# Kernel tuning notes

Measured on AMD Instinct MI355X. Metric: run time of the kernel, lower is better.

## Reference

```python
import jax, jax.numpy as jnp
import numpy as np

DIM = 1024; H = 16; DH = 64; L = 32; W = 8; E = 4  # ext_len = window_size//2
SEQ = 4096; B = 4
LN_EPS = 1e-5


def _ln(x, g, b):
    m = x.mean(-1, keepdims=True)
    v = ((x - m) ** 2).mean(-1, keepdims=True)
    return (x - m) / jnp.sqrt(v + LN_EPS) * g + b


def _split(x):  # (b,s,H*dh) -> (b,H,s,dh)
    b, s, _ = x.shape
    return x.reshape(b, s, H, DH).transpose(0, 2, 1, 3)


def _forward(query, Wq, bq, Wk, bk, Wv, bv, Wo, bo, g_l, b_l, g_s, b_s, Wd, bd):
    X = query.transpose(1, 0, 2)  # (b,s,d); s already multiple of W so no pad
    b, s, _ = X.shape
    Q = _split(X @ Wq + bq) * (1.0 / np.sqrt(DH))           # (b,H,s,dh)
    K = _split(_ln(X @ Wk + bk, g_l, b_l))
    V = _split(_ln(X @ Wv + bv, g_l, b_l))

    # landmark compression: softmax over sequence dim (no padding -> no mask)
    head_scores = jax.nn.softmax(X @ Wd + bd, axis=1)       # (b,s,H*L)
    hs = head_scores.reshape(b, s, H, L).transpose(0, 2, 3, 1)  # (b,H,L,s)
    Kc = jnp.einsum('bhls,bhsd->bhld', hs, K)
    Vc = jnp.einsum('bhls,bhsd->bhld', hs, V)
    # dual_ln_s applied over the flattened head dim, per landmark
    Kc = _split(_ln(Kc.transpose(0, 2, 1, 3).reshape(b, L, DIM), g_s, b_s))
    Vc = _split(_ln(Vc.transpose(0, 2, 1, 3).reshape(b, L, DIM), g_s, b_s))

    attn_compress = jnp.einsum('bhsd,bhld->bhsl', Q, Kc)    # (b,H,s,L)

    # sliding window band (v2): pad E on each side, tile into groups of W
    g = s // W
    band = W + 2 * E  # 16
    idx = jnp.arange(g)[:, None] * W + jnp.arange(band)[None, :]  # (g,band)
    K_pad = jnp.pad(K, ((0, 0), (0, 0), (E, E), (0, 0)))
    K_tiles = K_pad[:, :, idx, :]                           # (b,H,g,band,dh)
    Q_tiles = Q.reshape(b, H, g, W, DH)
    win = jnp.einsum('bhgwd,bhgkd->bhgwk', Q_tiles, K_tiles)
    valid = jnp.pad(jnp.ones((s,), bool), (E, E))[idx]      # (g,band) halo=False
    win = jnp.where(valid[None, None, :, None, :], win, -jnp.inf)
    win_flat = win.reshape(b, H, s, band)

    all_attn = jax.nn.softmax(jnp.concatenate([attn_compress, win_flat], -1), axis=-1)
    C = jnp.einsum('bhsl,bhld->bhsd', all_attn[..., :L], Vc)
    win_probs = all_attn[..., L:].reshape(b, H, g, W, band)
    V_pad = jnp.pad(V, ((0, 0), (0, 0), (E, E), (0, 0)))
    V_tiles = V_pad[:, :, idx, :]
    C = C + jnp.einsum('bhgwk,bhgkd->bhgwd', win_probs, V_tiles).reshape(b, H, s, DH)

    out = C.transpose(0, 2, 1, 3).reshape(b, s, DIM) @ Wo + bo
    return out.transpose(1, 0, 2)  # (s,b,d)


def setup_inputs() -> dict:
    key = jax.random.key(0)
    ks = jax.random.split(key, 7)
    sc = 0.02
    return {
        'query': jax.random.normal(ks[0], (SEQ, B, DIM), jnp.float32),
        'Wq': jax.random.normal(ks[1], (DIM, DIM), jnp.float32) * sc,
        'bq': jnp.zeros((DIM,), jnp.float32),
        'Wk': jax.random.normal(ks[2], (DIM, DIM), jnp.float32) * sc,
        'bk': jnp.zeros((DIM,), jnp.float32),
        'Wv': jax.random.normal(ks[3], (DIM, DIM), jnp.float32) * sc,
        'bv': jnp.zeros((DIM,), jnp.float32),
        'Wo': jax.random.normal(ks[4], (DIM, DIM), jnp.float32) * sc,
        'bo': jnp.zeros((DIM,), jnp.float32),
        'g_l': jnp.ones((DIM,), jnp.float32),
        'b_l': jnp.zeros((DIM,), jnp.float32),
        'g_s': jnp.ones((DIM,), jnp.float32),
        'b_s': jnp.zeros((DIM,), jnp.float32),
        'Wd': jax.random.normal(ks[5], (DIM, H * L), jnp.float32) * sc,
        'bd': jnp.zeros((H * L,), jnp.float32),
    }


def reference(query, Wq, bq, Wk, bk, Wv, bv, Wo, bo, g_l, b_l, g_s, b_s, Wd, bd):
    return _forward(query, Wq, bq, Wk, bk, Wv, bv, Wo, bo, g_l, b_l, g_s, b_s, Wd, bd)
```

## Files before the change

kernel.cpp:

```cpp
#include <hip/hip_runtime.h>
#include <cstddef>
#include <cstdint>

#define DIMC 1024
#define HC   16
#define DHC  64
#define LC   32
#define WC   8
#define EC   4
#define SEQC 4096
#define BC   4
#define MTOT 16384

typedef __attribute__((ext_vector_type(8))) __bf16 bf16x8;
typedef __attribute__((ext_vector_type(4))) float f32x4;

__device__ inline unsigned short f2b(float f) {
  unsigned int u = __float_as_uint(f);
  u += 0x7fff + ((u >> 16) & 1);
  return (unsigned short)(u >> 16);
}
__device__ inline float b2f(unsigned short u) {
  return __uint_as_float(((unsigned int)u) << 16);
}

__device__ inline void gll16(const void* g, void* l) {
  __builtin_amdgcn_global_load_lds(
      (__attribute__((address_space(1))) void*)g,
      (__attribute__((address_space(3))) void*)l, 16, 0, 0);
}

__global__ __launch_bounds__(256) void conv_rows(const float* __restrict__ src,
    unsigned short* __restrict__ dst) {
  int r = blockIdx.x;
  int sr = ((r & 4095) << 2) | (r >> 12);
  const float4* s = (const float4*)(src + (size_t)sr * 1024);
  ushort4* d = (ushort4*)(dst + (size_t)r * 1024);
  int t = threadIdx.x;
  float4 v = s[t];
  d[t] = make_ushort4(f2b(v.x), f2b(v.y), f2b(v.z), f2b(v.w));
}

__global__ __launch_bounds__(256) void conv_wT_all(
    const float* __restrict__ Wq, const float* __restrict__ Wk,
    const float* __restrict__ Wv, const float* __restrict__ Wd,
    const float* __restrict__ Wo, unsigned short* __restrict__ wAll,
    unsigned short* __restrict__ woT) {
  __shared__ float tile[32][33];
  int z = blockIdx.z;
  const float* W = (z == 0) ? Wq : (z == 1) ? Wk : (z == 2) ? Wv
                   : (z == 3) ? Wd : Wo;
  unsigned short* WT = (z == 4) ? woT : (wAll + (size_t)z * 1048576);
  int N = (z == 3) ? 512 : 1024;
  int n0 = blockIdx.x * 32, k0 = blockIdx.y * 32;
  if (n0 >= N) return;
  int t = threadIdx.x;
  int tr = t >> 5, tc = t & 31;
#pragma unroll
  for (int i = 0; i < 4; ++i)
    tile[tr + i * 8][tc] = W[(size_t)(k0 + tr + i * 8) * N + n0 + tc];
  __syncthreads();
#pragma unroll
  for (int i = 0; i < 4; ++i)
    WT[(size_t)(n0 + tr + i * 8) * 1024 + k0 + tc] = f2b(tile[tc][tr + i * 8]);
}

__global__ __launch_bounds__(512, 2) void gemm256(
    const unsigned short* __restrict__ A, const unsigned short* __restrict__ BT,
    const float* __restrict__ b0, const float* __restrict__ b1,
    const float* __restrict__ b2, const float* __restrict__ b3,
    unsigned short* __restrict__ o0, unsigned short* __restrict__ o1,
    unsigned short* __restrict__ o2, float* __restrict__ oy,
    float* __restrict__ outf, int mode) {
  extern __shared__ char smb[];
  unsigned short* smu = (unsigned short*)smb;
  int t = threadIdx.x;
  int w = t >> 6, lane = t & 63;
  int m = lane & 15, q4 = lane >> 4;
  int wr = (w >> 2) * 128, wc = (w & 3) * 64;
  int id = blockIdx.x;
  int xcd = id & 7, jj0 = id >> 3;
  int rowT = xcd * 8 + (jj0 & 7), colT = jj0 >> 3;
  int rowBase = rowT * 256, nBase = colT * 256;

  int srow = t >> 2;
  int gsw = ((t & 3) ^ ((t >> 3) & 3)) * 8;
  const unsigned short* gA0 = A + (size_t)(rowBase + srow) * 1024 + gsw;
  const unsigned short* gA1 = A + (size_t)(rowBase + 128 + srow) * 1024 + gsw;
  const unsigned short* gB0 = BT + (size_t)(nBase + srow) * 1024 + gsw;
  const unsigned short* gB1 = BT + (size_t)(nBase + 128 + srow) * 1024 + gsw;
  int ldsP0 = w * 1024;
  int ldsP1 = 8192 + w * 1024;
  int sx = (q4 ^ ((m >> 1) & 3)) * 8;
  f32x4 acc[8][4] = {};

#define STAGE5(kt_, c_)                                              \
  {                                                                  \
    int kc_ = (kt_) * 32;                                            \
    gll16(gA0 + kc_, smb + (c_)*16384 + ldsP0);                      \
    gll16(gA1 + kc_, smb + (c_)*16384 + ldsP1);                      \
    gll16(gB0 + kc_, smb + 32768 + (c_)*16384 + ldsP0);              \
    gll16(gB1 + kc_, smb + 32768 + (c_)*16384 + ldsP1);              \
  }

  STAGE5(0, 0);
  STAGE5(1, 1);
  asm volatile("s_waitcnt vmcnt(4)" ::: "memory");
  __builtin_amdgcn_s_barrier();
  __builtin_amdgcn_sched_barrier(0);

  for (int kt = 0; kt < 32; ++kt) {
    int c = kt & 1;
    const unsigned short* Au = smu + c * 8192;
    const unsigned short* Bu = smu + 16384 + c * 8192;
    bf16x8 bf[4];
#pragma unroll
    for (int jj = 0; jj < 4; ++jj)
      bf[jj] = *(const bf16x8*)(Bu + (wc + jj * 16 + m) * 32 + sx);
#pragma unroll
    for (int ip = 0; ip < 4; ++ip) {
      bf16x8 af0 = *(const bf16x8*)(Au + (wr + (ip * 2) * 16 + m) * 32 + sx);
      bf16x8 af1 =
          *(const bf16x8*)(Au + (wr + (ip * 2 + 1) * 16 + m) * 32 + sx);
      __builtin_amdgcn_s_setprio(1);
#pragma unroll
      for (int jj = 0; jj < 4; ++jj)
        acc[ip * 2][jj] = __builtin_amdgcn_mfma_f32_16x16x32_bf16(
            af0, bf[jj], acc[ip * 2][jj], 0, 0, 0);
#pragma unroll
      for (int jj = 0; jj < 4; ++jj)
        acc[ip * 2 + 1][jj] = __builtin_amdgcn_mfma_f32_16x16x32_bf16(
            af1, bf[jj], acc[ip * 2 + 1][jj], 0, 0, 0);
      __builtin_amdgcn_s_setprio(0);
    }
    if (kt == 31) break;
    __builtin_amdgcn_s_barrier();
    if (kt < 30) {
      STAGE5(kt + 2, c);
      asm volatile("s_waitcnt vmcnt(4)" ::: "memory");
    } else {
      asm volatile("s_waitcnt vmcnt(0)" ::: "memory");
    }
    __builtin_amdgcn_s_barrier();
    __builtin_amdgcn_sched_barrier(0);
  }
  __syncthreads();

  int segBase = nBase + wc;
  if (mode == 1) {
#pragma unroll
    for (int jj = 0; jj < 4; ++jj) {
      float bvv = b0[segBase + jj * 16 + m];
#pragma unroll
      for (int i = 0; i < 8; ++i)
#pragma unroll
        for (int r = 0; r < 4; ++r) {
          int rr = rowBase + wr + i * 16 + q4 * 4 + r;
          int orow = ((rr & 4095) << 2) | (rr >> 12);
          outf[(size_t)orow * 1024 + segBase + jj * 16 + m] =
              acc[i][jj][r] + bvv;
        }
    }
    return;
  }
  int seg = segBase >> 10;
  if (seg == 3) {
    int lc = segBase - 3072;
#pragma unroll
    for (int jj = 0; jj < 4; ++jj) {
      float bvv = b3[lc + jj * 16 + m];
#pragma unroll
      for (int i = 0; i < 8; ++i)
#pragma unroll
        for (int r = 0; r < 4; ++r)
          oy[(size_t)(rowBase + wr + i * 16 + q4 * 4 + r) * 512 + lc +
             jj * 16 + m] = acc[i][jj][r] + bvv;
    }
    return;
  }
  const float* bp = (seg == 0) ? b0 : (seg == 1) ? b1 : b2;
  unsigned short* ob = (seg == 0) ? o0 : (seg == 1) ? o1 : o2;
  float scl = (seg == 0) ? 0.125f : 1.0f;
  int lc0 = nBase & 1023;
#pragma unroll
  for (int h = 0; h < 2; ++h) {
    if ((w >> 2) == h) {
#pragma unroll
      for (int jj = 0; jj < 4; ++jj) {
        float bvv = bp[lc0 + wc + jj * 16 + m];
#pragma unroll
        for (int i = 0; i < 8; ++i)
#pragma unroll
          for (int r = 0; r < 4; ++r)
            smu[(i * 16 + q4 * 4 + r) * 264 + wc + jj * 16 + m] =
                f2b((acc[i][jj][r] + bvv) * scl);
      }
    }
    __syncthreads();
#pragma unroll
    for (int rd = 0; rd < 8; ++rd) {
      int idx = rd * 512 + t;
      int row = idx >> 5, cs = (idx & 31) * 8;
      uint4 v = *(const uint4*)(smu + row * 264 + cs);
      *(uint4*)(ob + (size_t)(rowBase + h * 128 + row) * 1024 + lc0 + cs) = v;
    }
    __syncthreads();
  }
}

__global__ __launch_bounds__(256) void ln_bf(unsigned short* __restrict__ buf,
    const float* __restrict__ g, const float* __restrict__ b) {
  int row = blockIdx.x;
  unsigned short* p = buf + (size_t)row * 1024;
  int tid = threadIdx.x;
  ushort4 u4 = ((const ushort4*)p)[tid];
  float x0 = b2f(u4.x), x1 = b2f(u4.y), x2 = b2f(u4.z), x3 = b2f(u4.w);
  float s = x0 + x1 + x2 + x3;
  float ss = x0 * x0 + x1 * x1 + x2 * x2 + x3 * x3;
#pragma unroll
  for (int off = 32; off > 0; off >>= 1) {
    s += __shfl_down(s, off);
    ss += __shfl_down(ss, off);
  }
  __shared__ float sred[8], ssred[8];
  int wave = tid >> 6, lane = tid & 63;
  if (lane == 0) { sred[wave] = s; ssred[wave] = ss; }
  __syncthreads();
  if (tid == 0) {
    float S = 0, SS = 0;
    for (int w = 0; w < 4; ++w) { S += sred[w]; SS += ssred[w]; }
    float m = S * (1.0f / 1024.0f);
    float v = SS * (1.0f / 1024.0f) - m * m;
    sred[0] = m;
    ssred[0] = rsqrtf(v + 1e-5f);
  }
  __syncthreads();
  float m = sred[0], rinv = ssred[0];
  float4 gg = ((const float4*)g)[tid];
  float4 bb = ((const float4*)b)[tid];
  ushort4 y;
  y.x = f2b((x0 - m) * rinv * gg.x + bb.x);
  y.y = f2b((x1 - m) * rinv * gg.y + bb.y);
  y.z = f2b((x2 - m) * rinv * gg.z + bb.z);
  y.w = f2b((x3 - m) * rinv * gg.w + bb.w);
  ((ushort4*)p)[tid] = y;
}

__global__ __launch_bounds__(256) void col_part(const float* __restrict__ yd,
    float* __restrict__ pm, float* __restrict__ ps) {
  int cg = blockIdx.x, b = blockIdx.y, sc = blockIdx.z;
  int t = threadIdx.x;
  int lane = t & 63, grp = t >> 6;
  const float* base = yd + (size_t)b * 4096 * 512 + (size_t)(sc * 256) * 512 +
                      cg * 64 + lane;
  float m = -1e30f, s = 0.f;
  for (int r = grp; r < 256; r += 4) {
    float x = base[(size_t)r * 512];
    float mn = fmaxf(m, x);
    s = s * expf(m - mn) + expf(x - mn);
    m = mn;
  }
  __shared__ float mS[4][64], sS[4][64];
  mS[grp][lane] = m;
  sS[grp][lane] = s;
  __syncthreads();
  if (grp == 0) {
    float M = mS[0][lane], S = sS[0][lane];
#pragma unroll
    for (int k = 1; k < 4; ++k) {
      float m2 = mS[k][lane], s2 = sS[k][lane];
      float Mn = fmaxf(M, m2);
      S = S * expf(M - Mn) + s2 * expf(m2 - Mn);
      M = Mn;
    }
    int col = cg * 64 + lane;
    pm[((size_t)(b * 512 + col)) * 16 + sc] = M;
    ps[((size_t)(b * 512 + col)) * 16 + sc] = S;
  }
}

__global__ __launch_bounds__(256) void col_combine(const float* __restrict__ pm,
    const float* __restrict__ ps, float* __restrict__ stats) {
  int idx = blockIdx.x * 256 + threadIdx.x;
  float M = -1e30f, S = 0.f;
#pragma unroll
  for (int sc = 0; sc < 16; ++sc) {
    float m2 = pm[(size_t)idx * 16 + sc], s2 = ps[(size_t)idx * 16 + sc];
    float Mn = fmaxf(M, m2);
    S = S * expf(M - Mn) + s2 * expf(m2 - Mn);
    M = Mn;
  }
  stats[(size_t)idx * 2] = M;
  stats[(size_t)idx * 2 + 1] = 1.0f / S;
}

#define NCHUNK 32
#define SCH    128
__global__ __launch_bounds__(256) void compress(const float* __restrict__ yd,
    const float* __restrict__ stats, const unsigned short* __restrict__ kbuf,
    const unsigned short* __restrict__ vbuf, float* __restrict__ kcp,
    float* __restrict__ vcp) {
  int c = blockIdx.x, h = blockIdx.y, b = blockIdx.z;
  int tid = threadIdx.x;
  int dq = tid & 15;
  int lp = tid >> 4;
  __shared__ float mxS[32], isS[32];
  __shared__ float pS[16][32];
  __shared__ float KfS[16][64];
  __shared__ float VfS[16][64];
  if (tid < 32) {
    mxS[tid] = stats[(size_t)(b * 512 + h * 32 + tid) * 2];
    isS[tid] = stats[(size_t)(b * 512 + h * 32 + tid) * 2 + 1];
  }
  __syncthreads();
  f32x4 aK0 = {}, aK1 = {}, aV0 = {}, aV1 = {};
  int s0 = c * SCH;
  for (int sc = 0; sc < SCH; sc += 16) {
    int bs = b * 4096 + s0 + sc;
    {
      int sl = tid >> 4;
      int l2 = (tid & 15) * 2;
      const float2 yv =
          *(const float2*)(yd + ((size_t)(bs + sl)) * 512 + h * 32 + l2);
      pS[sl][l2] = expf(yv.x - mxS[l2]) * isS[l2];
      pS[sl][l2 + 1] = expf(yv.y - mxS[l2 + 1]) * isS[l2 + 1];
      size_t roff = ((size_t)(bs + sl)) * 1024 + h * 64 + (tid & 15) * 4;
      ushort4 ku = *(const ushort4*)(kbuf + roff);
      ushort4 vu = *(const ushort4*)(vbuf + roff);
      f32x4 kf, vf;
      kf[0] = b2f(ku.x); kf[1] = b2f(ku.y); kf[2] = b2f(ku.z); kf[3] = b2f(ku.w);
      vf[0] = b2f(vu.x); vf[1] = b2f(vu.y); vf[2] = b2f(vu.z); vf[3] = b2f(vu.w);
      *(f32x4*)&KfS[sl][(tid & 15) * 4] = kf;
      *(f32x4*)&VfS[sl][(tid & 15) * 4] = vf;
    }
    __syncthreads();
#pragma unroll
    for (int sl = 0; sl < 16; ++sl) {
      float p0 = pS[sl][lp * 2];
      float p1 = pS[sl][lp * 2 + 1];
      const f32x4 kk = *(const f32x4*)&KfS[sl][dq * 4];
      const f32x4 vv = *(const f32x4*)&VfS[sl][dq * 4];
#pragma unroll
      for (int q = 0; q < 4; ++q) {
        aK0[q] += p0 * kk[q];
        aK1[q] += p1 * kk[q];
        aV0[q] += p0 * vv[q];
        aV1[q] += p1 * vv[q];
      }
    }
    __syncthreads();
  }
  size_t o0 = ((((size_t)c * 4 + b) * 16 + h) * 32 + (lp * 2)) * 64 + dq * 4;
  *(f32x4*)&kcp[o0] = aK0;
  *(f32x4*)&kcp[o0 + 64] = aK1;
  *(f32x4*)&vcp[o0] = aV0;
  *(f32x4*)&vcp[o0 + 64] = aV1;
}

__global__ __launch_bounds__(256) void ln_compress(const float* __restrict__ kcp,
    const float* __restrict__ vcp, const float* __restrict__ g_s,
    const float* __restrict__ b_s, float* __restrict__ kc_ln,
    float* __restrict__ vc_ln) {
  int row = blockIdx.x;
  int b = row >> 5, l = row & 31;
  const float* part = blockIdx.y ? vcp : kcp;
  float* outp = blockIdx.y ? vc_ln : kc_ln;
  int tid = threadIdx.x;
  int h = tid >> 4, d4 = (tid & 15) * 4;
  size_t base = (((size_t)b * 16 + h) * 32 + l) * 64 + d4;
  f32x4 x = {};
#pragma unroll
  for (int cch = 0; cch < NCHUNK; ++cch) {
    const f32x4 v = *(const f32x4*)&part[base + (size_t)cch * 131072];
#pragma unroll
    for (int q = 0; q < 4; ++q) x[q] += v[q];
  }
  float lsum = x[0] + x[1] + x[2] + x[3];
  float lss = x[0] * x[0] + x[1] * x[1] + x[2] * x[2] + x[3] * x[3];
#pragma unroll
  for (int off = 32; off > 0; off >>= 1) {
    lsum += __shfl_down(lsum, off);
    lss += __shfl_down(lss, off);
  }
  __shared__ float red[8], red2[8];
  int wave = tid >> 6, lane = tid & 63;
  if (lane == 0) { red[wave] = lsum; red2[wave] = lss; }
  __syncthreads();
  if (tid == 0) {
    float S = 0, SS = 0;
    for (int w = 0; w < 4; ++w) { S += red[w]; SS += red2[w]; }
    float m = S * (1.0f / 1024.0f);
    float v = SS * (1.0f / 1024.0f) - m * m;
    red[0] = m;
    red2[0] = rsqrtf(v + 1e-5f);
  }
  __syncthreads();
  float m = red[0], rinv = red2[0];
  int j = tid * 4;
  const float4 gg = *(const float4*)(g_s + j);
  const float4 bb = *(const float4*)(b_s + j);
  float4 yo;
  yo.x = (x[0] - m) * rinv * gg.x + bb.x;
  yo.y = (x[1] - m) * rinv * gg.y + bb.y;
  yo.z = (x[2] - m) * rinv * gg.z + bb.z;
  yo.w = (x[3] - m) * rinv * gg.w + bb.w;
  *(float4*)(outp + (size_t)row * 1024 + j) = yo;
}

__global__ __launch_bounds__(256) void attention(unsigned short* __restrict__ qc,
    const unsigned short* __restrict__ kbuf,
    const unsigned short* __restrict__ vbuf,
    const float* __restrict__ kc_ln, const float* __restrict__ vc_ln) {
  int qt = blockIdx.x, h = blockIdx.y, b = blockIdx.z;
  int t = threadIdx.x;
  int l = t & 63, w = t >> 6;
  int lr16 = l & 15, q4 = l >> 4;
  int s0 = qt * 64, hoff = h * 64;

  __shared__ unsigned short regionA[12672];
  __shared__ unsigned short Vt[64 * 128];
  unsigned short* Qs = regionA;
  unsigned short* Ks = regionA + 64 * 72;
  unsigned short* Ps = regionA;
  unsigned short* Cs = regionA + 64 * 128;

#pragma unroll
  for (int it = 0; it < 2; ++it) {
    int sid = it * 256 + t;
    int row = sid >> 3, seg = sid & 7;
    uint4 v = *(const uint4*)(qc + ((size_t)(b * 4096 + s0 + row)) * 1024 +
                              hoff + seg * 8);
    *(uint4*)(Qs + row * 72 + seg * 8) = v;
  }
#pragma unroll
  for (int it = 0; it < 2; ++it) {
    int sid = it * 256 + t;
    int row = sid >> 4, s4 = sid & 15;
    float4 v = *(const float4*)(kc_ln + ((size_t)(b * 32 + row)) * 1024 +
                                hoff + s4 * 4);
    ushort4 u = make_ushort4(f2b(v.x), f2b(v.y), f2b(v.z), f2b(v.w));
    *(ushort4*)(Ks + row * 72 + s4 * 4) = u;
  }
#pragma unroll
  for (int it = 0; it < 3; ++it) {
    int sid = it * 256 + t;
    if (sid < 576) {
      int r = sid >> 3, seg = sid & 7;
      int pos = s0 - 4 + r;
      uint4 v = {0, 0, 0, 0};
      if (pos >= 0 && pos < 4096)
        v = *(const uint4*)(kbuf + ((size_t)(b * 4096 + pos)) * 1024 + hoff +
                            seg * 8);
      *(uint4*)(Ks + (32 + r) * 72 + seg * 8) = v;
    }
  }
#pragma unroll
  for (int it = 0; it < 8; ++it) {
    int d = t & 63;
    int k0 = (t >> 6) * 4 + it * 16;
    unsigned short vv[4];
#pragma unroll
    for (int i = 0; i < 4; ++i) {
      int kk = k0 + i;
      unsigned short x = 0;
      if (kk < 32) {
        x = f2b(vc_ln[((size_t)(b * 32 + kk)) * 1024 + hoff + d]);
      } else if (kk < 104) {
        int pos = s0 - 4 + (kk - 32);
        if (pos >= 0 && pos < 4096)
          x = vbuf[((size_t)(b * 4096 + pos)) * 1024 + hoff + d];
      }
      vv[i] = x;
    }
    *(ushort4*)(Vt + d * 128 + (k0 ^ ((d & 31) << 2))) = *(ushort4*)vv;
  }
  __syncthreads();

  int mbase = w * 16;
  bf16x8 aq[2];
#pragma unroll
  for (int ks = 0; ks < 2; ++ks)
    aq[ks] = *(const bf16x8*)(Qs + (mbase + lr16) * 72 + ks * 32 + q4 * 8);
  f32x4 S[7];
#pragma unroll
  for (int nb = 0; nb < 7; ++nb) {
    f32x4 acc = {};
#pragma unroll
    for (int ks = 0; ks < 2; ++ks) {
      bf16x8 bk =
          *(const bf16x8*)(Ks + (nb * 16 + lr16) * 72 + ks * 32 + q4 * 8);
      acc = __builtin_amdgcn_mfma_f32_16x16x32_bf16(aq[ks], bk, acc, 0, 0, 0);
    }
    S[nb] = acc;
  }

  float ex[7][4];
#pragma unroll
  for (int r = 0; r < 4; ++r) {
    int qrow = mbase + q4 * 4 + r;
    int g8 = (qrow >> 3) * 8;
    float m = -1e30f;
#pragma unroll
    for (int nb = 0; nb < 7; ++nb) {
      int col = nb * 16 + lr16;
      float v = S[nb][r];
      if (col >= 32) {
        int rw = col - 32;
        int pos = s0 - 4 + rw;
        bool ok = (rw >= g8) && (rw < g8 + 16) && (pos >= 0) && (pos < 4096);
        if (!ok) v = -INFINITY;
      }
      ex[nb][r] = v;
      m = fmaxf(m, v);
    }
    m = fmaxf(m, __shfl_xor(m, 1));
    m = fmaxf(m, __shfl_xor(m, 2));
    m = fmaxf(m, __shfl_xor(m, 4));
    m = fmaxf(m, __shfl_xor(m, 8));
    float s = 0.f;
#pragma unroll
    for (int nb = 0; nb < 7; ++nb) {
      float e = expf(ex[nb][r] - m);
      ex[nb][r] = e;
      s += e;
    }
    s += __shfl_xor(s, 1);
    s += __shfl_xor(s, 2);
    s += __shfl_xor(s, 4);
    s += __shfl_xor(s, 8);
    float inv = 1.0f / s;
#pragma unroll
    for (int nb = 0; nb < 7; ++nb) ex[nb][r] *= inv;
  }
  __syncthreads();

  if (t < 128) {
    int q = t >> 1, blk = 14 + (t & 1);
    uint4 z = {0, 0, 0, 0};
    *(uint4*)(Ps + q * 128 + ((blk ^ (q & 7)) << 3)) = z;
  }
#pragma unroll
  for (int r = 0; r < 4; ++r) {
    int q = mbase + q4 * 4 + r;
#pragma unroll
    for (int nb = 0; nb < 7; ++nb) {
      int col = nb * 16 + lr16;
      int blk = col >> 3;
      Ps[q * 128 + ((blk ^ (q & 7)) << 3) + (col & 7)] = f2b(ex[nb][r]);
    }
  }
  __syncthreads();

  bf16x8 pa[4];
#pragma unroll
  for (int ks = 0; ks < 4; ++ks) {
    int q = mbase + lr16;
    int blk = ks * 4 + q4;
    pa[ks] = *(const bf16x8*)(Ps + q * 128 + ((blk ^ (q & 7)) << 3));
  }
#pragma unroll
  for (int nb = 0; nb < 4; ++nb) {
    f32x4 acc = {};
    int d = nb * 16 + lr16;
#pragma unroll
    for (int ks = 0; ks < 4; ++ks) {
      unsigned short vv[8];
#pragma unroll
      for (int jh = 0; jh < 2; ++jh) {
        int k4 = ks * 32 + q4 * 8 + jh * 4;
        *(ushort4*)(vv + jh * 4) =
            *(const ushort4*)(Vt + d * 128 + (k4 ^ ((d & 31) << 2)));
      }
      acc = __builtin_amdgcn_mfma_f32_16x16x32_bf16(pa[ks], *(const bf16x8*)vv,
                                                    acc, 0, 0, 0);
    }
#pragma unroll
    for (int r = 0; r < 4; ++r) {
      int row = mbase + q4 * 4 + r;
      Cs[row * 68 + d] = f2b(acc[r]);
    }
  }
  __syncthreads();

#pragma unroll
  for (int it = 0; it < 2; ++it) {
    int sid = it * 256 + t;
    int row = sid >> 3, seg = sid & 7;
    ushort4 a0 = *(const ushort4*)(Cs + row * 68 + seg * 8);
    ushort4 a1 = *(const ushort4*)(Cs + row * 68 + seg * 8 + 4);
    unsigned short u[8];
    *(ushort4*)u = a0;
    *(ushort4*)(u + 4) = a1;
    *(uint4*)(qc + ((size_t)(b * 4096 + s0 + row)) * 1024 + hoff + seg * 8) =
        *(uint4*)u;
  }
}

extern "C" void kernel_launch(void* const* d_in, const int* in_sizes, int n_in,
                              void* d_out, int out_size, void* d_ws,
                              size_t ws_size, hipStream_t stream) {
  const float* query = (const float*)d_in[0];
  const float* Wq = (const float*)d_in[1];
  const float* bq = (const float*)d_in[2];
  const float* Wk = (const float*)d_in[3];
  const float* bk = (const float*)d_in[4];
  const float* Wv = (const float*)d_in[5];
  const float* bv = (const float*)d_in[6];
  const float* Wo = (const float*)d_in[7];
  const float* bo = (const float*)d_in[8];
  const float* g_l = (const float*)d_in[9];
  const float* b_l = (const float*)d_in[10];
  const float* g_s = (const float*)d_in[11];
  const float* b_s = (const float*)d_in[12];
  const float* Wd = (const float*)d_in[13];
  const float* bd = (const float*)d_in[14];
  float* out = (float*)d_out;

  static bool attr_set = []() {
    hipFuncSetAttribute((const void*)gemm256,
                        hipFuncAttributeMaxDynamicSharedMemorySize, 135168);
    return true;
  }();
  (void)attr_set;

  unsigned short* qb = (unsigned short*)d_ws;
  unsigned short* kb = qb + 16777216;
  unsigned short* vb = kb + 16777216;
  unsigned short* xb = vb + 16777216;
  float* yd = (float*)(xb + 16777216);
  float* stats = yd + 8388608;
  float* col_pm = stats + 4096;
  float* col_ps = col_pm + 32768;
  float* kc_part = col_ps + 32768;
  float* vc_part = kc_part + 4194304;
  float* kc_ln = vc_part + 4194304;
  float* vc_ln = kc_ln + 131072;
  unsigned short* wAll = (unsigned short*)(vc_ln + 131072);
  unsigned short* woT = wAll + 3670016;

  dim3 blk(256);
  conv_rows<<<16384, blk, 0, stream>>>(query, xb);
  conv_wT_all<<<dim3(32, 32, 5), blk, 0, stream>>>(Wq, Wk, Wv, Wd, Wo,
                                                   wAll, woT);
  gemm256<<<896, dim3(512), 67584, stream>>>(xb, wAll, bq, bk, bv, bd,
                                             qb, kb, vb, yd, nullptr, 0);
  ln_bf<<<32768, blk, 0, stream>>>(kb, g_l, b_l);
  col_part<<<dim3(8, 4, 16), blk, 0, stream>>>(yd, col_pm, col_ps);
  col_combine<<<8, blk, 0, stream>>>(col_pm, col_ps, stats);
  compress<<<dim3(NCHUNK, 16, 4), blk, 0, stream>>>(yd, stats, kb, vb,
                                                    kc_part, vc_part);
  ln_compress<<<dim3(128, 2), blk, 0, stream>>>(kc_part, vc_part, g_s, b_s,
                                                kc_ln, vc_ln);
  attention<<<dim3(64, 16, 4), blk, 0, stream>>>(qb, kb, vb, kc_ln, vc_ln);
  gemm256<<<256, dim3(512), 67584, stream>>>(qb, woT, bo, nullptr, nullptr,
                                             nullptr, nullptr, nullptr,
                                             nullptr, nullptr, out, 1);
}
```

Measured before the change: 521.7 us.

## Shrink GEMM tile to 256x128 with triple-buffered LDS pipeline

Changes the bf16 MFMA GEMM from 256x256 tiles to 256x128 tiles, giving each wave a 64x64 sub-tile and doubling the grid size. It raises launch bounds to 4 blocks per CU and replaces double buffering with a three-stage LDS ring, issuing the next loads before compute and dropping one barrier per k-step. The aim is more occupancy and better latency hiding. In exchange, each block reuses less data, so total global traffic per FLOP goes up, and the epilogue now uses a single LDS pass.

```diff
diff --git a/kernel.cpp b/kernel.cpp
--- a/kernel.cpp
+++ b/kernel.cpp
@@ -65,7 +65,7 @@
     WT[(size_t)(n0 + tr + i * 8) * 1024 + k0 + tc] = f2b(tile[tc][tr + i * 8]);
 }
 
-__global__ __launch_bounds__(512, 2) void gemm256(
+__global__ __launch_bounds__(512, 4) void gemm128(
     const unsigned short* __restrict__ A, const unsigned short* __restrict__ BT,
     const float* __restrict__ b0, const float* __restrict__ b1,
     const float* __restrict__ b2, const float* __restrict__ b3,
@@ -77,67 +77,59 @@
   int t = threadIdx.x;
   int w = t >> 6, lane = t & 63;
   int m = lane & 15, q4 = lane >> 4;
-  int wr = (w >> 2) * 128, wc = (w & 3) * 64;
+  int wr = (w >> 1) * 64, wc = (w & 1) * 64;
   int id = blockIdx.x;
-  int xcd = id & 7, jj0 = id >> 3;
-  int rowT = xcd * 8 + (jj0 & 7), colT = jj0 >> 3;
-  int rowBase = rowT * 256, nBase = colT * 256;
+  int rowT = (id & 7) * 8 + ((id >> 3) & 7);
+  int colT = id >> 6;
+  int rowBase = rowT * 256, nBase = colT * 128;
 
   int srow = t >> 2;
   int gsw = ((t & 3) ^ ((t >> 3) & 3)) * 8;
   const unsigned short* gA0 = A + (size_t)(rowBase + srow) * 1024 + gsw;
   const unsigned short* gA1 = A + (size_t)(rowBase + 128 + srow) * 1024 + gsw;
   const unsigned short* gB0 = BT + (size_t)(nBase + srow) * 1024 + gsw;
-  const unsigned short* gB1 = BT + (size_t)(nBase + 128 + srow) * 1024 + gsw;
-  int ldsP0 = w * 1024;
-  int ldsP1 = 8192 + w * 1024;
+  int ldsW = w * 1024;
   int sx = (q4 ^ ((m >> 1) & 3)) * 8;
-  f32x4 acc[8][4] = {};
-
-#define STAGE5(kt_, c_)                                              \
-  {                                                                  \
-    int kc_ = (kt_) * 32;                                            \
-    gll16(gA0 + kc_, smb + (c_)*16384 + ldsP0);                      \
-    gll16(gA1 + kc_, smb + (c_)*16384 + ldsP1);                      \
-    gll16(gB0 + kc_, smb + 32768 + (c_)*16384 + ldsP0);              \
-    gll16(gB1 + kc_, smb + 32768 + (c_)*16384 + ldsP1);              \
-  }
-
-  STAGE5(0, 0);
-  STAGE5(1, 1);
-  asm volatile("s_waitcnt vmcnt(4)" ::: "memory");
+  f32x4 acc[4][4] = {};
+
+#define STAGE7(kt_, c_)                                          \
+  {                                                              \
+    int kc_ = (kt_) * 32;                                        \
+    gll16(gA0 + kc_, smb + (c_) * 24576 + ldsW);                 \
+    gll16(gA1 + kc_, smb + (c_) * 24576 + 8192 + ldsW);          \
+    gll16(gB0 + kc_, smb + (c_) * 24576 + 16384 + ldsW);         \
+  }
+
+  STAGE7(0, 0);
+  STAGE7(1, 1);
+  asm volatile("s_waitcnt vmcnt(3)" ::: "memory");
   __builtin_amdgcn_s_barrier();
   __builtin_amdgcn_sched_barrier(0);
 
   for (int kt = 0; kt < 32; ++kt) {
-    int c = kt & 1;
-    const unsigned short* Au = smu + c * 8192;
-    const unsigned short* Bu = smu + 16384 + c * 8192;
-    bf16x8 bf[4];
+    int c = kt % 3;
+    if (kt < 30) STAGE7(kt + 2, (kt + 2) % 3);
+    const unsigned short* Au = smu + c * 12288;
+    const unsigned short* Bu = smu + c * 12288 + 8192;
+    bf16x8 bfB[4];
 #pragma unroll
     for (int jj = 0; jj < 4; ++jj)
-      bf[jj] = *(const bf16x8*)(Bu + (wc + jj * 16 + m) * 32 + sx);
-#pragma unroll
-    for (int ip = 0; ip < 4; ++ip) {
-      bf16x8 af0 = *(const bf16x8*)(Au + (wr + (ip * 2) * 16 + m) * 32 + sx);
-      bf16x8 af1 =
-          *(const bf16x8*)(Au + (wr + (ip * 2 + 1) * 16 + m) * 32 + sx);
-      __builtin_amdgcn_s_setprio(1);
+      bfB[jj] = *(const bf16x8*)(Bu + (wc + jj * 16 + m) * 32 + sx);
+    bf16x8 afA[4];
+#pragma unroll
+    for (int mi = 0; mi < 4; ++mi)
+      afA[mi] = *(const bf16x8*)(Au + (wr + mi * 16 + m) * 32 + sx);
+    __builtin_amdgcn_s_setprio(1);
+#pragma unroll
+    for (int mi = 0; mi < 4; ++mi)
 #pragma unroll
       for (int jj = 0; jj < 4; ++jj)
-        acc[ip * 2][jj] = __builtin_amdgcn_mfma_f32_16x16x32_bf16(
-            af0, bf[jj], acc[ip * 2][jj], 0, 0, 0);
-#pragma unroll
-      for (int jj = 0; jj < 4; ++jj)
-        acc[ip * 2 + 1][jj] = __builtin_amdgcn_mfma_f32_16x16x32_bf16(
-            af1, bf[jj], acc[ip * 2 + 1][jj], 0, 0, 0);
-      __builtin_amdgcn_s_setprio(0);
-    }
+        acc[mi][jj] = __builtin_amdgcn_mfma_f32_16x16x32_bf16(
+            afA[mi], bfB[jj], acc[mi][jj], 0, 0, 0);
+    __builtin_amdgcn_s_setprio(0);
     if (kt == 31) break;
-    __builtin_amdgcn_s_barrier();
     if (kt < 30) {
-      STAGE5(kt + 2, c);
-      asm volatile("s_waitcnt vmcnt(4)" ::: "memory");
+      asm volatile("s_waitcnt vmcnt(3)" ::: "memory");
     } else {
       asm volatile("s_waitcnt vmcnt(0)" ::: "memory");
     }
@@ -146,35 +138,34 @@
   }
   __syncthreads();
 
-  int segBase = nBase + wc;
   if (mode == 1) {
 #pragma unroll
     for (int jj = 0; jj < 4; ++jj) {
-      float bvv = b0[segBase + jj * 16 + m];
-#pragma unroll
-      for (int i = 0; i < 8; ++i)
+      int col = nBase + wc + jj * 16 + m;
+      float bvv = b0[col];
+#pragma unroll
+      for (int mi = 0; mi < 4; ++mi)
 #pragma unroll
         for (int r = 0; r < 4; ++r) {
-          int rr = rowBase + wr + i * 16 + q4 * 4 + r;
+          int rr = rowBase + wr + mi * 16 + q4 * 4 + r;
           int orow = ((rr & 4095) << 2) | (rr >> 12);
-          outf[(size_t)orow * 1024 + segBase + jj * 16 + m] =
-              acc[i][jj][r] + bvv;
+          outf[(size_t)orow * 1024 + col] = acc[mi][jj][r] + bvv;
         }
     }
     return;
   }
-  int seg = segBase >> 10;
+  int seg = nBase >> 10;
   if (seg == 3) {
-    int lc = segBase - 3072;
+    int lc0 = nBase - 3072;
 #pragma unroll
     for (int jj = 0; jj < 4; ++jj) {
-      float bvv = b3[lc + jj * 16 + m];
-#pragma unroll
-      for (int i = 0; i < 8; ++i)
+      float bvv = b3[lc0 + wc + jj * 16 + m];
+#pragma unroll
+      for (int mi = 0; mi < 4; ++mi)
 #pragma unroll
         for (int r = 0; r < 4; ++r)
-          oy[(size_t)(rowBase + wr + i * 16 + q4 * 4 + r) * 512 + lc +
-             jj * 16 + m] = acc[i][jj][r] + bvv;
+          oy[(size_t)(rowBase + wr + mi * 16 + q4 * 4 + r) * 512 + lc0 + wc +
+             jj * 16 + m] = acc[mi][jj][r] + bvv;
     }
     return;
   }
@@ -183,28 +174,22 @@
   float scl = (seg == 0) ? 0.125f : 1.0f;
   int lc0 = nBase & 1023;
 #pragma unroll
-  for (int h = 0; h < 2; ++h) {
-    if ((w >> 2) == h) {
-#pragma unroll
-      for (int jj = 0; jj < 4; ++jj) {
-        float bvv = bp[lc0 + wc + jj * 16 + m];
-#pragma unroll
-        for (int i = 0; i < 8; ++i)
-#pragma unroll
-          for (int r = 0; r < 4; ++r)
-            smu[(i * 16 + q4 * 4 + r) * 264 + wc + jj * 16 + m] =
-                f2b((acc[i][jj][r] + bvv) * scl);
-      }
-    }
-    __syncthreads();
-#pragma unroll
-    for (int rd = 0; rd < 8; ++rd) {
-      int idx = rd * 512 + t;
-      int row = idx >> 5, cs = (idx & 31) * 8;
-      uint4 v = *(const uint4*)(smu + row * 264 + cs);
-      *(uint4*)(ob + (size_t)(rowBase + h * 128 + row) * 1024 + lc0 + cs) = v;
-    }
-    __syncthreads();
+  for (int jj = 0; jj < 4; ++jj) {
+    float bvv = bp[lc0 + wc + jj * 16 + m];
+#pragma unroll
+    for (int mi = 0; mi < 4; ++mi)
+#pragma unroll
+      for (int r = 0; r < 4; ++r)
+        smu[(wr + mi * 16 + q4 * 4 + r) * 136 + wc + jj * 16 + m] =
+            f2b((acc[mi][jj][r] + bvv) * scl);
+  }
+  __syncthreads();
+#pragma unroll
+  for (int rd = 0; rd < 8; ++rd) {
+    int idx = rd * 512 + t;
+    int row = idx >> 4, cs = (idx & 15) * 8;
+    uint4 v = *(const uint4*)(smu + row * 136 + cs);
+    *(uint4*)(ob + (size_t)(rowBase + row) * 1024 + lc0 + cs) = v;
   }
 }
 
@@ -617,8 +602,8 @@
   float* out = (float*)d_out;
 
   static bool attr_set = []() {
-    hipFuncSetAttribute((const void*)gemm256,
-                        hipFuncAttributeMaxDynamicSharedMemorySize, 135168);
+    hipFuncSetAttribute((const void*)gemm128,
+                        hipFuncAttributeMaxDynamicSharedMemorySize, 73728);
     return true;
   }();
   (void)attr_set;
@@ -642,8 +627,8 @@
   conv_rows<<<16384, blk, 0, stream>>>(query, xb);
   conv_wT_all<<<dim3(32, 32, 5), blk, 0, stream>>>(Wq, Wk, Wv, Wd, Wo,
                                                    wAll, woT);
-  gemm256<<<896, dim3(512), 67584, stream>>>(xb, wAll, bq, bk, bv, bd,
-                                             qb, kb, vb, yd, nullptr, 0);
+  gemm128<<<1792, dim3(512), 73728, stream>>>(xb, wAll, bq, bk, bv, bd,
+                                              qb, kb, vb, yd, nullptr, 0);
   ln_bf<<<32768, blk, 0, stream>>>(kb, g_l, b_l);
   col_part<<<dim3(8, 4, 16), blk, 0, stream>>>(yd, col_pm, col_ps);
   col_combine<<<8, blk, 0, stream>>>(col_pm, col_ps, stats);
@@ -652,7 +637,7 @@
   ln_compress<<<dim3(128, 2), blk, 0, stream>>>(kc_part, vc_part, g_s, b_s,
                                                 kc_ln, vc_ln);
   attention<<<dim3(64, 16, 4), blk, 0, stream>>>(qb, kb, vb, kc_ln, vc_ln);
-  gemm256<<<256, dim3(512), 67584, stream>>>(qb, woT, bo, nullptr, nullptr,
+  gemm128<<<512, dim3(512), 73728, stream>>>(qb, woT, bo, nullptr, nullptr,
                                              nullptr, nullptr, nullptr,
                                              nullptr, nullptr, out, 1);
 }
```

After: 493.4 us. 1.06x faster.
